# Optimization experiments

Measured on AMD Instinct MI355X. Metric: run time of the kernel, lower is better.

Reference implementation:

```python
import jax, jax.numpy as jnp
from jax import lax
import numpy as np

B, L, D = 4, 4096, 1024
H = 16
HD = D // H          # 64
WIN = 256
NC = L // WIN
N_ITER = 50          # entmax-bisect iterations (entmax library default)
LN_EPS = 1e-5


def _p(x, am1):
    # clamp(x, min=0) ** (1/(alpha-1))
    return jnp.clip(x, 0.0) ** (1.0 / am1)


def entmax_bisect(X, alpha):
    """alpha-entmax along the last axis via bisection. alpha broadcastable to X."""
    am1 = alpha - 1.0
    Xs = X * am1
    d = X.shape[-1]
    max_val = Xs.max(axis=-1, keepdims=True)
    tau_lo = max_val - 1.0                       # 1 ** (alpha-1)
    tau_hi = max_val - (1.0 / d) ** am1
    f_lo = _p(Xs - tau_lo, am1).sum(-1, keepdims=True) - 1.0
    dm0 = tau_hi - tau_lo

    def body(i, carry):
        tau_lo, dm, _ = carry
        dm = dm * 0.5
        tau_m = tau_lo + dm
        f_m = _p(Xs - tau_m, am1).sum(-1, keepdims=True) - 1.0
        tau_lo = jnp.where(f_m * f_lo >= 0, tau_m, tau_lo)
        return (tau_lo, dm, tau_m)

    tau_lo, dm, tau_m = lax.fori_loop(0, N_ITER, body, (tau_lo, dm0, tau_lo))
    p = _p(Xs - tau_m, am1)
    return p / p.sum(-1, keepdims=True)          # ensure_sum_one


def setup_inputs() -> dict:
    key = jax.random.key(0)
    ks = jax.random.split(key, 4)
    x = jax.random.normal(ks[0], (B, L, D), jnp.float32)
    alpha = jnp.full((H,), 1.5, jnp.float32)
    qkv_w = 0.02 * jax.random.normal(ks[1], (3 * D, D), jnp.float32)
    qkv_b = jnp.zeros((3 * D,), jnp.float32)
    o_w = 0.02 * jax.random.normal(ks[2], (D, D), jnp.float32)
    o_b = jnp.zeros((D,), jnp.float32)
    ln_gamma = jnp.ones((D,), jnp.float32)
    ln_beta = jnp.zeros((D,), jnp.float32)
    return {"x": x, "alpha": alpha, "qkv_w": qkv_w, "qkv_b": qkv_b,
            "o_w": o_w, "o_b": o_b, "ln_gamma": ln_gamma, "ln_beta": ln_beta}


def reference(x, alpha, qkv_w, qkv_b, o_w, o_b, ln_gamma, ln_beta):
    # qkv projection -> [B, H, L, 3*HD]
    qkv = (x @ qkv_w.T + qkv_b).reshape(B, L, H, 3 * HD).transpose(0, 2, 1, 3)
    q, k, v = jnp.split(qkv, 3, axis=-1)
    # block-diagonal windows (span=None => k/v chunks coincide with q chunks)
    qc = q.reshape(B, H, NC, WIN, HD)
    kc = k.reshape(B, H, NC, WIN, HD)
    vc = v.reshape(B, H, NC, WIN, HD)
    scores = jnp.einsum('bhcqd,bhckd->bhcqk', qc, kc) / np.sqrt(HD).astype(np.float32)
    weights = entmax_bisect(scores, alpha.reshape(1, H, 1, 1, 1))
    out = jnp.einsum('bhcqk,bhckd->bhcqd', weights, vc)
    out = out.reshape(B, H, L, HD).transpose(0, 2, 1, 3).reshape(B, L, D)
    # layer norm
    mu = out.mean(-1, keepdims=True)
    var = out.var(-1, keepdims=True)
    out = (out - mu) * lax.rsqrt(var + LN_EPS) * ln_gamma + ln_beta
    return out @ o_w.T + o_b
```

## Files before the change

### kernel.cpp

```cpp
#include <hip/hip_runtime.h>

typedef unsigned short u16;
typedef unsigned int   u32;
typedef __attribute__((ext_vector_type(8))) short bf16x8;
typedef __attribute__((ext_vector_type(4))) float f32x4;
typedef __attribute__((ext_vector_type(8))) u16  u16x8;

__device__ __forceinline__ float b2f(u16 u) {
    union { u32 i; float f; } v; v.i = ((u32)u) << 16; return v.f;
}
__device__ __forceinline__ u16 f2b(float f) {
    u32 i = __float_as_uint(f);
    u32 r = (i + 0x7FFFu + ((i >> 16) & 1u)) >> 16;
    return (u16)r;
}
__device__ __forceinline__ bool is_bf16(const u32* gprobe) { return *gprobe == 0x3F803F80u; }

__device__ __forceinline__ void load_lds16(const void* g, void* l) {
    __builtin_amdgcn_global_load_lds((__attribute__((address_space(1))) void*)g,
                                     (__attribute__((address_space(3))) void*)l, 16, 0, 0);
}

__global__ __launch_bounds__(256) void cvt_kern(const void* __restrict__ src, u16* __restrict__ dst,
                                                int n8, const u32* __restrict__ gprobe) {
    const bool isb = is_bf16(gprobe);
    const int i = blockIdx.x * 256 + threadIdx.x;
    if (i >= n8) return;
    if (isb) {
        ((u16x8*)dst)[i] = ((const u16x8*)src)[i];
    } else {
        const float* s = (const float*)src + (size_t)i * 8;
        u16x8 o;
        #pragma unroll
        for (int j = 0; j < 8; j++) o[j] = f2b(s[j]);
        ((u16x8*)dst)[i] = o;
    }
}

__global__ __launch_bounds__(256) void gemm_bt(const u16* __restrict__ A, const u16* __restrict__ B,
                                               const void* __restrict__ bias,
                                               u16* __restrict__ Cb, float* __restrict__ Cf,
                                               const u32* __restrict__ gprobe, int out_mode,
                                               int M, int N, int K) {
    __shared__ u16 lsA[128 * 32];
    __shared__ u16 lsB[128 * 32];
    const int tid  = threadIdx.x;
    const int wave = tid >> 6, lane = tid & 63;
    const int m0 = blockIdx.y * 128, n0 = blockIdx.x * 128;
    const int wr = wave >> 1, wc = wave & 1;

    f32x4 acc[4][4] = {};

    const int srow = wave * 16 + (lane >> 2);
    const int scol = (lane & 3) * 8;
    const u16* gA0 = A + (size_t)(m0 + srow) * K + scol;
    const u16* gB0 = B + (size_t)(n0 + srow) * K + scol;
    u16* lA0 = &lsA[wave * 512];
    u16* lB0 = &lsB[wave * 512];
    const size_t rstep = (size_t)64 * K;

    for (int k0 = 0; k0 < K; k0 += 32) {
        __syncthreads();
        load_lds16(gA0 + k0,         lA0);
        load_lds16(gA0 + k0 + rstep, lA0 + 2048);
        load_lds16(gB0 + k0,         lB0);
        load_lds16(gB0 + k0 + rstep, lB0 + 2048);
        __syncthreads();

        bf16x8 af[4], bfr[4];
        #pragma unroll
        for (int mi = 0; mi < 4; mi++)
            af[mi] = *(const bf16x8*)&lsA[(wr * 64 + mi * 16 + (lane & 15)) * 32 + (lane >> 4) * 8];
        #pragma unroll
        for (int ni = 0; ni < 4; ni++)
            bfr[ni] = *(const bf16x8*)&lsB[(wc * 64 + ni * 16 + (lane & 15)) * 32 + (lane >> 4) * 8];
        #pragma unroll
        for (int mi = 0; mi < 4; mi++)
            #pragma unroll
            for (int ni = 0; ni < 4; ni++)
                acc[mi][ni] = __builtin_amdgcn_mfma_f32_16x16x32_bf16(af[mi], bfr[ni], acc[mi][ni], 0, 0, 0);
    }

    const bool isb     = is_bf16(gprobe);
    const bool store_b = (out_mode == 0) || isb;
    const int g = lane >> 4, cc = lane & 15;
    #pragma unroll
    for (int ni = 0; ni < 4; ni++) {
        const int col = n0 + wc * 64 + ni * 16 + cc;
        const float bv = isb ? b2f(((const u16*)bias)[col]) : ((const float*)bias)[col];
        #pragma unroll
        for (int mi = 0; mi < 4; mi++) {
            const int row = m0 + wr * 64 + mi * 16 + g * 4;
            #pragma unroll
            for (int i = 0; i < 4; i++) {
                const float v = acc[mi][ni][i] + bv;
                const size_t idx = (size_t)(row + i) * N + col;
                if (store_b) Cb[idx] = f2b(v);
                else         Cf[idx] = v;
            }
        }
    }
}

__device__ __forceinline__ void bfly_sum4(float (&a)[4]) {
    #pragma unroll
    for (int m = 1; m <= 8; m <<= 1)
        #pragma unroll
        for (int i = 0; i < 4; i++) a[i] += __shfl_xor(a[i], m, 64);
}

__device__ __forceinline__ void entmax2_rows(f32x4 (&s)[16]) {
    float mx[4] = {-3e38f, -3e38f, -3e38f, -3e38f};
    #pragma unroll
    for (int nt = 0; nt < 16; nt++)
        #pragma unroll
        for (int i = 0; i < 4; i++) mx[i] = fmaxf(mx[i], s[nt][i]);
    #pragma unroll
    for (int m = 1; m <= 8; m <<= 1)
        #pragma unroll
        for (int i = 0; i < 4; i++) mx[i] = fmaxf(mx[i], __shfl_xor(mx[i], m, 64));

    float tau[4];
    #pragma unroll
    for (int i = 0; i < 4; i++) tau[i] = mx[i] - 1.0f;

    #pragma unroll 1
    for (int it = 0; it < 10; it++) {
        float a2[4] = {0.f, 0.f, 0.f, 0.f};
        float a1[4] = {0.f, 0.f, 0.f, 0.f};
        #pragma unroll
        for (int nt = 0; nt < 16; nt++)
            #pragma unroll
            for (int i = 0; i < 4; i++) {
                float t = fmaxf(s[nt][i] - tau[i], 0.0f);
                a2[i] = fmaf(t, t, a2[i]);
                a1[i] += t;
            }
        bfly_sum4(a2);
        bfly_sum4(a1);
        #pragma unroll
        for (int i = 0; i < 4; i++)
            tau[i] += (a2[i] - 1.0f) * 0.5f * __builtin_amdgcn_rcpf(a1[i]);
    }

    float ss[4] = {0.f, 0.f, 0.f, 0.f};
    #pragma unroll
    for (int nt = 0; nt < 16; nt++)
        #pragma unroll
        for (int i = 0; i < 4; i++) {
            float t = fmaxf(s[nt][i] - tau[i], 0.0f);
            float p = t * t;
            s[nt][i] = p;
            ss[i] += p;
        }
    bfly_sum4(ss);
    float inv[4];
    #pragma unroll
    for (int i = 0; i < 4; i++) inv[i] = 1.0f / ss[i];
    #pragma unroll
    for (int nt = 0; nt < 16; nt++)
        #pragma unroll
        for (int i = 0; i < 4; i++) s[nt][i] *= inv[i];
}

__device__ __forceinline__ void entmax_gen_rows(f32x4 (&s)[16], float e, float dm0) {
    float mx[4] = {-3e38f, -3e38f, -3e38f, -3e38f};
    #pragma unroll
    for (int nt = 0; nt < 16; nt++)
        #pragma unroll
        for (int i = 0; i < 4; i++) mx[i] = fmaxf(mx[i], s[nt][i]);
    #pragma unroll
    for (int m = 1; m <= 8; m <<= 1)
        #pragma unroll
        for (int i = 0; i < 4; i++) mx[i] = fmaxf(mx[i], __shfl_xor(mx[i], m, 64));

    float tau_lo[4], tau_m[4], f_lo[4];
    #pragma unroll
    for (int i = 0; i < 4; i++) { tau_lo[i] = mx[i] - 1.0f; tau_m[i] = tau_lo[i]; }
    {
        float a[4] = {0.f, 0.f, 0.f, 0.f};
        #pragma unroll
        for (int nt = 0; nt < 16; nt++)
            #pragma unroll
            for (int i = 0; i < 4; i++) {
                float t = fmaxf(s[nt][i] - tau_lo[i], 0.0f);
                a[i] += (t > 0.0f) ? __expf(e * __logf(t)) : 0.0f;
            }
        bfly_sum4(a);
        #pragma unroll
        for (int i = 0; i < 4; i++) f_lo[i] = a[i] - 1.0f;
    }
    float dm = dm0;
    #pragma unroll 1
    for (int it = 0; it < 26; it++) {
        dm *= 0.5f;
        #pragma unroll
        for (int i = 0; i < 4; i++) tau_m[i] = tau_lo[i] + dm;
        float a[4] = {0.f, 0.f, 0.f, 0.f};
        #pragma unroll
        for (int nt = 0; nt < 16; nt++)
            #pragma unroll
            for (int i = 0; i < 4; i++) {
                float t = fmaxf(s[nt][i] - tau_m[i], 0.0f);
                a[i] += (t > 0.0f) ? __expf(e * __logf(t)) : 0.0f;
            }
        bfly_sum4(a);
        #pragma unroll
        for (int i = 0; i < 4; i++)
            tau_lo[i] = ((a[i] - 1.0f) * f_lo[i] >= 0.0f) ? tau_m[i] : tau_lo[i];
    }
    float ss[4] = {0.f, 0.f, 0.f, 0.f};
    #pragma unroll
    for (int nt = 0; nt < 16; nt++)
        #pragma unroll
        for (int i = 0; i < 4; i++) {
            float t = fmaxf(s[nt][i] - tau_m[i], 0.0f);
            float p = (t > 0.0f) ? __expf(e * __logf(t)) : 0.0f;
            s[nt][i] = p;
            ss[i] += p;
        }
    bfly_sum4(ss);
    float inv[4];
    #pragma unroll
    for (int i = 0; i < 4; i++) inv[i] = 1.0f / ss[i];
    #pragma unroll
    for (int nt = 0; nt < 16; nt++)
        #pragma unroll
        for (int i = 0; i < 4; i++) s[nt][i] *= inv[i];
}

template<bool SQ>
__global__ __launch_bounds__(256, 2) void attn_win_t(const u16* __restrict__ qkv,
                                                     const void* __restrict__ alpha, u16* __restrict__ att,
                                                     const u32* __restrict__ gprobe) {
    __shared__ u16 Kl[256 * 64];
    __shared__ u16 Vt[64 * 256];
    __shared__ u16 Wl[4 * 16 * 64];
    const int tid  = threadIdx.x;
    const int wave = tid >> 6, lane = tid & 63;
    const int c = blockIdx.x, h = blockIdx.y, b = blockIdx.z;
    const int g = lane >> 4, cc = lane & 15;

    const float av  = is_bf16(gprobe) ? b2f(((const u16*)alpha)[h]) : ((const float*)alpha)[h];
    const float am1 = av - 1.0f;
    const float e   = 1.0f / am1;
    const bool  sq  = (e == 2.0f);
    if (SQ != sq) return;
    const float scl = am1 * 0.125f;

    const size_t tok0 = (size_t)b * 4096 + (size_t)c * 256;
    const u16* qbase = qkv + tok0 * 3072 + h * 192;
    const u16* kbase = qbase + 64;
    const u16* vbase = qbase + 128;
    char* wl = (char*)&Wl[wave * (16 * 64)];

    {
        const int kr = tid >> 3, kc2 = tid & 7;
        #pragma unroll
        for (int it = 0; it < 8; it++) {
            const int row = it * 32 + kr;
            bf16x8 kv = *(const bf16x8*)(kbase + (size_t)row * 3072 + kc2 * 8);
            const int off = (row * 128 + kc2 * 16) ^ ((row & 7) << 4);
            *(bf16x8*)((char*)Kl + off) = kv;
        }
    }

    {
        const int d = tid & 63, tg = tid >> 6;
        #pragma unroll
        for (int j = 0; j < 8; j++) {
            const int t0 = tg * 64 + j * 8;
            u16x8 tmp;
            #pragma unroll
            for (int i = 0; i < 8; i++)
                tmp[i] = vbase[(size_t)(t0 + i) * 3072 + d];
            const int off = (d * 512 + t0 * 2) ^ ((d & 7) << 4);
            *(u16x8*)((char*)Vt + off) = tmp;
        }
    }
    __syncthreads();

    for (int ch = 0; ch < 4; ch++) {
        const int r0 = ch * 64 + wave * 16;

        const u16* qr = qbase + (size_t)(r0 + cc) * 3072 + g * 8;
        bf16x8 q0 = *(const bf16x8*)qr;
        bf16x8 q1 = *(const bf16x8*)(qr + 32);

        f32x4 s[16] = {};
        #pragma unroll
        for (int nt = 0; nt < 16; nt++) {
            const int krow = nt * 16 + cc;
            const int swz  = (cc & 7) << 4;
            const int off0 = (krow * 128 + g * 16) ^ swz;
            const int off1 = (krow * 128 + g * 16 + 64) ^ swz;
            bf16x8 bk0 = *(const bf16x8*)((const char*)Kl + off0);
            bf16x8 bk1 = *(const bf16x8*)((const char*)Kl + off1);
            s[nt] = __builtin_amdgcn_mfma_f32_16x16x32_bf16(q0, bk0, s[nt], 0, 0, 0);
            s[nt] = __builtin_amdgcn_mfma_f32_16x16x32_bf16(q1, bk1, s[nt], 0, 0, 0);
        }
        #pragma unroll
        for (int nt = 0; nt < 16; nt++)
            #pragma unroll
            for (int i = 0; i < 4; i++) s[nt][i] *= scl;

        if constexpr (SQ) {
            entmax2_rows(s);
        } else {
            const float dm0 = 1.0f - exp2f(-8.0f * am1);
            entmax_gen_rows(s, e, dm0);
        }

        f32x4 o[4] = {};
        #pragma unroll
        for (int kc = 0; kc < 8; kc++) {
            #pragma unroll
            for (int t = 0; t < 2; t++) {
                const int nt = kc * 2 + t;
                #pragma unroll
                for (int i = 0; i < 4; i++) {
                    const int wrow = g * 4 + i;
                    const int off  = (wrow * 128 + t * 32 + cc * 2) ^ ((wrow & 7) << 4);
                    *(u16*)(wl + off) = f2b(s[nt][i]);
                }
            }
            bf16x8 aw = *(const bf16x8*)(wl + ((cc * 128 + g * 16) ^ ((cc & 7) << 4)));
            #pragma unroll
            for (int nd = 0; nd < 4; nd++) {
                const int vrow = nd * 16 + cc;
                const int voff = (vrow * 512 + kc * 64 + g * 16) ^ ((cc & 7) << 4);
                bf16x8 bv = *(const bf16x8*)((const char*)Vt + voff);
                o[nd] = __builtin_amdgcn_mfma_f32_16x16x32_bf16(aw, bv, o[nd], 0, 0, 0);
            }
        }

        #pragma unroll
        for (int nd = 0; nd < 4; nd++)
            #pragma unroll
            for (int i = 0; i < 4; i++) {
                const int wrow = g * 4 + i;
                const int off  = (wrow * 128 + nd * 32 + cc * 2) ^ ((wrow & 7) << 4);
                *(u16*)(wl + off) = f2b(o[nd][i]);
            }
        #pragma unroll
        for (int p = 0; p < 2; p++) {
            const int row = p * 8 + (lane >> 3);
            const int off = (row * 128 + (lane & 7) * 16) ^ ((row & 7) << 4);
            u16x8 val = *(const u16x8*)(wl + off);
            *(u16x8*)(att + (size_t)(tok0 + r0 + row) * 1024 + h * 64 + (lane & 7) * 8) = val;
        }
    }
}

__global__ __launch_bounds__(256) void ln_kern(const u16* __restrict__ att, const void* __restrict__ gam,
                                               const void* __restrict__ bet, u16* __restrict__ out,
                                               const u32* __restrict__ gprobe) {
    const bool isb = is_bf16(gprobe);
    const int tid = threadIdx.x;
    const int wave = tid >> 6, lane = tid & 63;
    const size_t tok = (size_t)blockIdx.x * 4 + wave;
    const u16* p = att + tok * 1024 + lane * 16;
    u16x8 v0 = *(const u16x8*)p;
    u16x8 v1 = *(const u16x8*)(p + 8);
    float x[16];
    #pragma unroll
    for (int j = 0; j < 8; j++) { x[j] = b2f(v0[j]); x[j + 8] = b2f(v1[j]); }
    float s = 0.f, s2 = 0.f;
    #pragma unroll
    for (int j = 0; j < 16; j++) { s += x[j]; s2 = fmaf(x[j], x[j], s2); }
    #pragma unroll
    for (int m = 1; m <= 32; m <<= 1) { s += __shfl_xor(s, m, 64); s2 += __shfl_xor(s2, m, 64); }
    const float mean = s * (1.0f / 1024.0f);
    const float var  = s2 * (1.0f / 1024.0f) - mean * mean;
    const float rs   = rsqrtf(var + 1e-5f);

    float gv[16], bv[16];
    if (isb) {
        const u16* gp = (const u16*)gam + lane * 16;
        const u16* bp = (const u16*)bet + lane * 16;
        u16x8 g0 = *(const u16x8*)gp, g1 = *(const u16x8*)(gp + 8);
        u16x8 b0 = *(const u16x8*)bp, b1 = *(const u16x8*)(bp + 8);
        #pragma unroll
        for (int j = 0; j < 8; j++) {
            gv[j] = b2f(g0[j]); gv[j + 8] = b2f(g1[j]);
            bv[j] = b2f(b0[j]); bv[j + 8] = b2f(b1[j]);
        }
    } else {
        const float* gp = (const float*)gam + lane * 16;
        const float* bp = (const float*)bet + lane * 16;
        #pragma unroll
        for (int j = 0; j < 16; j++) { gv[j] = gp[j]; bv[j] = bp[j]; }
    }

    u16x8 w0, w1;
    #pragma unroll
    for (int j = 0; j < 8; j++) {
        w0[j] = f2b((x[j]     - mean) * rs * gv[j]     + bv[j]);
        w1[j] = f2b((x[j + 8] - mean) * rs * gv[j + 8] + bv[j + 8]);
    }
    u16* op = out + tok * 1024 + lane * 16;
    *(u16x8*)op       = w0;
    *(u16x8*)(op + 8) = w1;
}

extern "C" void kernel_launch(void* const* d_in, const int* in_sizes, int n_in,
                              void* d_out, int out_size, void* d_ws, size_t ws_size,
                              hipStream_t stream) {
    const void* x      = d_in[0];
    const void* alpha  = d_in[1];
    const void* qkv_w  = d_in[2];
    const void* qkv_b  = d_in[3];
    const void* o_w    = d_in[4];
    const void* o_b    = d_in[5];
    const u32*  gprobe = (const u32*)d_in[6];
    const void* gam    = d_in[6];
    const void* bet    = d_in[7];

    u16* xb  = (u16*)d_ws;
    u16* wq  = xb + (size_t)16384 * 1024;
    u16* wo  = wq + (size_t)3072 * 1024;
    u16* qkv = wo + (size_t)1024 * 1024;
    u16* att = (u16*)d_out;
    u16* ln  = xb;

    dim3 blk(256);
    cvt_kern<<<dim3((16384 * 1024 / 8 + 255) / 256), blk, 0, stream>>>(x, xb, 16384 * 1024 / 8, gprobe);
    cvt_kern<<<dim3((3072 * 1024 / 8 + 255) / 256), blk, 0, stream>>>(qkv_w, wq, 3072 * 1024 / 8, gprobe);
    cvt_kern<<<dim3((1024 * 1024 / 8 + 255) / 256), blk, 0, stream>>>(o_w, wo, 1024 * 1024 / 8, gprobe);
    gemm_bt<<<dim3(3072 / 128, 16384 / 128), blk, 0, stream>>>(xb, wq, qkv_b, qkv, nullptr, gprobe, 0,
                                                               16384, 3072, 1024);
    attn_win_t<true ><<<dim3(16, 16, 4), blk, 0, stream>>>(qkv, alpha, att, gprobe);
    attn_win_t<false><<<dim3(16, 16, 4), blk, 0, stream>>>(qkv, alpha, att, gprobe);
    ln_kern<<<dim3(4096), blk, 0, stream>>>(att, gam, bet, ln, gprobe);
    gemm_bt<<<dim3(1024 / 128, 16384 / 128), blk, 0, stream>>>(ln, wo, o_b, (u16*)d_out, (float*)d_out,
                                                               gprobe, 1, 16384, 1024, 1024);
}
```

Baseline: 547.2 us.

## Split attention window columns across waves with LDS cross-wave entmax reductions

Restructures the windowed attention kernel so each wave owns a 64-key slice of the window, with K held in registers instead of LDS. All four waves process the same 16 query rows together, and the entmax row reductions (max, Newton or bisection sums, normalisation) are combined across waves through small double-buffered LDS arrays with block barriers. This cuts the per-wave register footprint (scores shrink from 16 to 4 tiles) and LDS use, allowing three blocks per CU. The cost is a __syncthreads on every entmax iteration, about 10 per row tile for alpha=1.5 and 27 for general alpha, plus narrower output stores.

```diff
diff --git a/kernel.cpp b/kernel.cpp
--- a/kernel.cpp
+++ b/kernel.cpp
@@ -5,6 +5,7 @@
 typedef __attribute__((ext_vector_type(8))) short bf16x8;
 typedef __attribute__((ext_vector_type(4))) float f32x4;
 typedef __attribute__((ext_vector_type(8))) u16  u16x8;
+typedef __attribute__((ext_vector_type(4))) u16  u16x4;
 
 __device__ __forceinline__ float b2f(u16 u) {
     union { u32 i; float f; } v; v.i = ((u32)u) << 16; return v.f;
@@ -108,134 +109,24 @@
         #pragma unroll
         for (int i = 0; i < 4; i++) a[i] += __shfl_xor(a[i], m, 64);
 }
-
-__device__ __forceinline__ void entmax2_rows(f32x4 (&s)[16]) {
-    float mx[4] = {-3e38f, -3e38f, -3e38f, -3e38f};
-    #pragma unroll
-    for (int nt = 0; nt < 16; nt++)
-        #pragma unroll
-        for (int i = 0; i < 4; i++) mx[i] = fmaxf(mx[i], s[nt][i]);
+__device__ __forceinline__ void bfly_max4(float (&a)[4]) {
     #pragma unroll
     for (int m = 1; m <= 8; m <<= 1)
         #pragma unroll
-        for (int i = 0; i < 4; i++) mx[i] = fmaxf(mx[i], __shfl_xor(mx[i], m, 64));
-
-    float tau[4];
-    #pragma unroll
-    for (int i = 0; i < 4; i++) tau[i] = mx[i] - 1.0f;
-
-    #pragma unroll 1
-    for (int it = 0; it < 10; it++) {
-        float a2[4] = {0.f, 0.f, 0.f, 0.f};
-        float a1[4] = {0.f, 0.f, 0.f, 0.f};
-        #pragma unroll
-        for (int nt = 0; nt < 16; nt++)
-            #pragma unroll
-            for (int i = 0; i < 4; i++) {
-                float t = fmaxf(s[nt][i] - tau[i], 0.0f);
-                a2[i] = fmaf(t, t, a2[i]);
-                a1[i] += t;
-            }
-        bfly_sum4(a2);
-        bfly_sum4(a1);
-        #pragma unroll
-        for (int i = 0; i < 4; i++)
-            tau[i] += (a2[i] - 1.0f) * 0.5f * __builtin_amdgcn_rcpf(a1[i]);
-    }
-
-    float ss[4] = {0.f, 0.f, 0.f, 0.f};
-    #pragma unroll
-    for (int nt = 0; nt < 16; nt++)
-        #pragma unroll
-        for (int i = 0; i < 4; i++) {
-            float t = fmaxf(s[nt][i] - tau[i], 0.0f);
-            float p = t * t;
-            s[nt][i] = p;
-            ss[i] += p;
-        }
-    bfly_sum4(ss);
-    float inv[4];
-    #pragma unroll
-    for (int i = 0; i < 4; i++) inv[i] = 1.0f / ss[i];
-    #pragma unroll
-    for (int nt = 0; nt < 16; nt++)
-        #pragma unroll
-        for (int i = 0; i < 4; i++) s[nt][i] *= inv[i];
-}
-
-__device__ __forceinline__ void entmax_gen_rows(f32x4 (&s)[16], float e, float dm0) {
-    float mx[4] = {-3e38f, -3e38f, -3e38f, -3e38f};
-    #pragma unroll
-    for (int nt = 0; nt < 16; nt++)
-        #pragma unroll
-        for (int i = 0; i < 4; i++) mx[i] = fmaxf(mx[i], s[nt][i]);
-    #pragma unroll
-    for (int m = 1; m <= 8; m <<= 1)
-        #pragma unroll
-        for (int i = 0; i < 4; i++) mx[i] = fmaxf(mx[i], __shfl_xor(mx[i], m, 64));
-
-    float tau_lo[4], tau_m[4], f_lo[4];
-    #pragma unroll
-    for (int i = 0; i < 4; i++) { tau_lo[i] = mx[i] - 1.0f; tau_m[i] = tau_lo[i]; }
-    {
-        float a[4] = {0.f, 0.f, 0.f, 0.f};
-        #pragma unroll
-        for (int nt = 0; nt < 16; nt++)
-            #pragma unroll
-            for (int i = 0; i < 4; i++) {
-                float t = fmaxf(s[nt][i] - tau_lo[i], 0.0f);
-                a[i] += (t > 0.0f) ? __expf(e * __logf(t)) : 0.0f;
-            }
-        bfly_sum4(a);
-        #pragma unroll
-        for (int i = 0; i < 4; i++) f_lo[i] = a[i] - 1.0f;
-    }
-    float dm = dm0;
-    #pragma unroll 1
-    for (int it = 0; it < 26; it++) {
-        dm *= 0.5f;
-        #pragma unroll
-        for (int i = 0; i < 4; i++) tau_m[i] = tau_lo[i] + dm;
-        float a[4] = {0.f, 0.f, 0.f, 0.f};
-        #pragma unroll
-        for (int nt = 0; nt < 16; nt++)
-            #pragma unroll
-            for (int i = 0; i < 4; i++) {
-                float t = fmaxf(s[nt][i] - tau_m[i], 0.0f);
-                a[i] += (t > 0.0f) ? __expf(e * __logf(t)) : 0.0f;
-            }
-        bfly_sum4(a);
-        #pragma unroll
-        for (int i = 0; i < 4; i++)
-            tau_lo[i] = ((a[i] - 1.0f) * f_lo[i] >= 0.0f) ? tau_m[i] : tau_lo[i];
-    }
-    float ss[4] = {0.f, 0.f, 0.f, 0.f};
-    #pragma unroll
-    for (int nt = 0; nt < 16; nt++)
-        #pragma unroll
-        for (int i = 0; i < 4; i++) {
-            float t = fmaxf(s[nt][i] - tau_m[i], 0.0f);
-            float p = (t > 0.0f) ? __expf(e * __logf(t)) : 0.0f;
-            s[nt][i] = p;
-            ss[i] += p;
-        }
-    bfly_sum4(ss);
-    float inv[4];
-    #pragma unroll
-    for (int i = 0; i < 4; i++) inv[i] = 1.0f / ss[i];
-    #pragma unroll
-    for (int nt = 0; nt < 16; nt++)
-        #pragma unroll
-        for (int i = 0; i < 4; i++) s[nt][i] *= inv[i];
+        for (int i = 0; i < 4; i++) a[i] = fmaxf(a[i], __shfl_xor(a[i], m, 64));
 }
 
 template<bool SQ>
-__global__ __launch_bounds__(256, 2) void attn_win_t(const u16* __restrict__ qkv,
+__global__ __launch_bounds__(256, 3) void attn_win_t(const u16* __restrict__ qkv,
                                                      const void* __restrict__ alpha, u16* __restrict__ att,
                                                      const u32* __restrict__ gprobe) {
-    __shared__ u16 Kl[256 * 64];
     __shared__ u16 Vt[64 * 256];
-    __shared__ u16 Wl[4 * 16 * 64];
+    __shared__ u16 Wb[16 * 264];
+    __shared__ u16 Ob[16 * 72];
+    __shared__ f32x4 redM[4][4];
+    __shared__ f32x4 redA[2][4][4];
+    __shared__ f32x4 redB[2][4][4];
+
     const int tid  = threadIdx.x;
     const int wave = tid >> 6, lane = tid & 63;
     const int c = blockIdx.x, h = blockIdx.y, b = blockIdx.z;
@@ -252,18 +143,6 @@
     const u16* qbase = qkv + tok0 * 3072 + h * 192;
     const u16* kbase = qbase + 64;
     const u16* vbase = qbase + 128;
-    char* wl = (char*)&Wl[wave * (16 * 64)];
-
-    {
-        const int kr = tid >> 3, kc2 = tid & 7;
-        #pragma unroll
-        for (int it = 0; it < 8; it++) {
-            const int row = it * 32 + kr;
-            bf16x8 kv = *(const bf16x8*)(kbase + (size_t)row * 3072 + kc2 * 8);
-            const int off = (row * 128 + kc2 * 16) ^ ((row & 7) << 4);
-            *(bf16x8*)((char*)Kl + off) = kv;
-        }
-    }
 
     {
         const int d = tid & 63, tg = tid >> 6;
@@ -278,76 +157,220 @@
             *(u16x8*)((char*)Vt + off) = tmp;
         }
     }
+
+    bf16x8 kf0[4], kf1[4];
+    #pragma unroll
+    for (int nt = 0; nt < 4; nt++) {
+        const u16* kr = kbase + (size_t)(wave * 64 + nt * 16 + cc) * 3072 + g * 8;
+        kf0[nt] = *(const bf16x8*)kr;
+        kf1[nt] = *(const bf16x8*)(kr + 32);
+    }
     __syncthreads();
 
-    for (int ch = 0; ch < 4; ch++) {
-        const int r0 = ch * 64 + wave * 16;
+    int buf = 0;
+    #pragma unroll 1
+    for (int ci = 0; ci < 16; ci++) {
+        const int r0 = ci * 16;
 
         const u16* qr = qbase + (size_t)(r0 + cc) * 3072 + g * 8;
         bf16x8 q0 = *(const bf16x8*)qr;
         bf16x8 q1 = *(const bf16x8*)(qr + 32);
 
-        f32x4 s[16] = {};
-        #pragma unroll
-        for (int nt = 0; nt < 16; nt++) {
-            const int krow = nt * 16 + cc;
-            const int swz  = (cc & 7) << 4;
-            const int off0 = (krow * 128 + g * 16) ^ swz;
-            const int off1 = (krow * 128 + g * 16 + 64) ^ swz;
-            bf16x8 bk0 = *(const bf16x8*)((const char*)Kl + off0);
-            bf16x8 bk1 = *(const bf16x8*)((const char*)Kl + off1);
-            s[nt] = __builtin_amdgcn_mfma_f32_16x16x32_bf16(q0, bk0, s[nt], 0, 0, 0);
-            s[nt] = __builtin_amdgcn_mfma_f32_16x16x32_bf16(q1, bk1, s[nt], 0, 0, 0);
-        }
-        #pragma unroll
-        for (int nt = 0; nt < 16; nt++)
+        f32x4 s[4] = {};
+        #pragma unroll
+        for (int nt = 0; nt < 4; nt++) {
+            s[nt] = __builtin_amdgcn_mfma_f32_16x16x32_bf16(q0, kf0[nt], s[nt], 0, 0, 0);
+            s[nt] = __builtin_amdgcn_mfma_f32_16x16x32_bf16(q1, kf1[nt], s[nt], 0, 0, 0);
+        }
+        #pragma unroll
+        for (int nt = 0; nt < 4; nt++)
             #pragma unroll
             for (int i = 0; i < 4; i++) s[nt][i] *= scl;
 
+        float mx[4] = {-3e38f, -3e38f, -3e38f, -3e38f};
+        #pragma unroll
+        for (int nt = 0; nt < 4; nt++)
+            #pragma unroll
+            for (int i = 0; i < 4; i++) mx[i] = fmaxf(mx[i], s[nt][i]);
+        bfly_max4(mx);
+        if (cc == 0) {
+            f32x4 t; t[0] = mx[0]; t[1] = mx[1]; t[2] = mx[2]; t[3] = mx[3];
+            redM[wave][g] = t;
+        }
+        __syncthreads();
+        float rm[4];
+        {
+            f32x4 m0 = redM[0][g], m1 = redM[1][g], m2 = redM[2][g], m3 = redM[3][g];
+            #pragma unroll
+            for (int i = 0; i < 4; i++) rm[i] = fmaxf(fmaxf(m0[i], m1[i]), fmaxf(m2[i], m3[i]));
+        }
+
         if constexpr (SQ) {
-            entmax2_rows(s);
+            float tau[4];
+            #pragma unroll
+            for (int i = 0; i < 4; i++) tau[i] = rm[i] - 1.0f;
+            #pragma unroll 1
+            for (int it = 0; it < 10; it++) {
+                float a2[4] = {0.f, 0.f, 0.f, 0.f};
+                float a1[4] = {0.f, 0.f, 0.f, 0.f};
+                #pragma unroll
+                for (int nt = 0; nt < 4; nt++)
+                    #pragma unroll
+                    for (int i = 0; i < 4; i++) {
+                        float t = fmaxf(s[nt][i] - tau[i], 0.0f);
+                        a2[i] = fmaf(t, t, a2[i]);
+                        a1[i] += t;
+                    }
+                bfly_sum4(a2);
+                bfly_sum4(a1);
+                if (cc == 0) {
+                    f32x4 t2; t2[0] = a2[0]; t2[1] = a2[1]; t2[2] = a2[2]; t2[3] = a2[3];
+                    f32x4 t1; t1[0] = a1[0]; t1[1] = a1[1]; t1[2] = a1[2]; t1[3] = a1[3];
+                    redA[buf][wave][g] = t2;
+                    redB[buf][wave][g] = t1;
+                }
+                __syncthreads();
+                {
+                    f32x4 A0 = redA[buf][0][g], A1v = redA[buf][1][g], A2v = redA[buf][2][g], A3 = redA[buf][3][g];
+                    f32x4 B0 = redB[buf][0][g], B1v = redB[buf][1][g], B2v = redB[buf][2][g], B3 = redB[buf][3][g];
+                    #pragma unroll
+                    for (int i = 0; i < 4; i++) {
+                        const float A2s = (A0[i] + A1v[i]) + (A2v[i] + A3[i]);
+                        const float A1s = (B0[i] + B1v[i]) + (B2v[i] + B3[i]);
+                        tau[i] += (A2s - 1.0f) * 0.5f * __builtin_amdgcn_rcpf(A1s);
+                    }
+                }
+                buf ^= 1;
+            }
+            float ss[4] = {0.f, 0.f, 0.f, 0.f};
+            #pragma unroll
+            for (int nt = 0; nt < 4; nt++)
+                #pragma unroll
+                for (int i = 0; i < 4; i++) {
+                    float t = fmaxf(s[nt][i] - tau[i], 0.0f);
+                    float p = t * t;
+                    s[nt][i] = p;
+                    ss[i] += p;
+                }
+            bfly_sum4(ss);
+            if (cc == 0) {
+                f32x4 t; t[0] = ss[0]; t[1] = ss[1]; t[2] = ss[2]; t[3] = ss[3];
+                redA[buf][wave][g] = t;
+            }
+            __syncthreads();
+            {
+                f32x4 S0 = redA[buf][0][g], S1 = redA[buf][1][g], S2 = redA[buf][2][g], S3 = redA[buf][3][g];
+                #pragma unroll
+                for (int i = 0; i < 4; i++) {
+                    const float inv = 1.0f / ((S0[i] + S1[i]) + (S2[i] + S3[i]));
+                    #pragma unroll
+                    for (int nt = 0; nt < 4; nt++) s[nt][i] *= inv;
+                }
+            }
+            buf ^= 1;
         } else {
             const float dm0 = 1.0f - exp2f(-8.0f * am1);
-            entmax_gen_rows(s, e, dm0);
-        }
-
-        f32x4 o[4] = {};
-        #pragma unroll
-        for (int kc = 0; kc < 8; kc++) {
-            #pragma unroll
-            for (int t = 0; t < 2; t++) {
-                const int nt = kc * 2 + t;
+            float tau_lo[4], tau_m[4], f_lo[4];
+            #pragma unroll
+            for (int i = 0; i < 4; i++) { tau_lo[i] = rm[i] - 1.0f; tau_m[i] = tau_lo[i]; }
+            {
+                float a[4] = {0.f, 0.f, 0.f, 0.f};
+                #pragma unroll
+                for (int nt = 0; nt < 4; nt++)
+                    #pragma unroll
+                    for (int i = 0; i < 4; i++) {
+                        float t = fmaxf(s[nt][i] - tau_lo[i], 0.0f);
+                        a[i] += (t > 0.0f) ? __expf(e * __logf(t)) : 0.0f;
+                    }
+                bfly_sum4(a);
+                if (cc == 0) {
+                    f32x4 t; t[0] = a[0]; t[1] = a[1]; t[2] = a[2]; t[3] = a[3];
+                    redA[buf][wave][g] = t;
+                }
+                __syncthreads();
+                f32x4 S0 = redA[buf][0][g], S1 = redA[buf][1][g], S2 = redA[buf][2][g], S3 = redA[buf][3][g];
+                #pragma unroll
+                for (int i = 0; i < 4; i++) f_lo[i] = (S0[i] + S1[i]) + (S2[i] + S3[i]) - 1.0f;
+                buf ^= 1;
+            }
+            float dm = dm0;
+            #pragma unroll 1
+            for (int it = 0; it < 26; it++) {
+                dm *= 0.5f;
+                #pragma unroll
+                for (int i = 0; i < 4; i++) tau_m[i] = tau_lo[i] + dm;
+                float a[4] = {0.f, 0.f, 0.f, 0.f};
+                #pragma unroll
+                for (int nt = 0; nt < 4; nt++)
+                    #pragma unroll
+                    for (int i = 0; i < 4; i++) {
+                        float t = fmaxf(s[nt][i] - tau_m[i], 0.0f);
+                        a[i] += (t > 0.0f) ? __expf(e * __logf(t)) : 0.0f;
+                    }
+                bfly_sum4(a);
+                if (cc == 0) {
+                    f32x4 t; t[0] = a[0]; t[1] = a[1]; t[2] = a[2]; t[3] = a[3];
+                    redA[buf][wave][g] = t;
+                }
+                __syncthreads();
+                f32x4 S0 = redA[buf][0][g], S1 = redA[buf][1][g], S2 = redA[buf][2][g], S3 = redA[buf][3][g];
+                #pragma unroll
+                for (int i = 0; i < 4; i++)
+                    tau_lo[i] = (((S0[i] + S1[i]) + (S2[i] + S3[i]) - 1.0f) * f_lo[i] >= 0.0f) ? tau_m[i] : tau_lo[i];
+                buf ^= 1;
+            }
+            float ss[4] = {0.f, 0.f, 0.f, 0.f};
+            #pragma unroll
+            for (int nt = 0; nt < 4; nt++)
                 #pragma unroll
                 for (int i = 0; i < 4; i++) {
-                    const int wrow = g * 4 + i;
-                    const int off  = (wrow * 128 + t * 32 + cc * 2) ^ ((wrow & 7) << 4);
-                    *(u16*)(wl + off) = f2b(s[nt][i]);
-                }
-            }
-            bf16x8 aw = *(const bf16x8*)(wl + ((cc * 128 + g * 16) ^ ((cc & 7) << 4)));
-            #pragma unroll
-            for (int nd = 0; nd < 4; nd++) {
-                const int vrow = nd * 16 + cc;
-                const int voff = (vrow * 512 + kc * 64 + g * 16) ^ ((cc & 7) << 4);
-                bf16x8 bv = *(const bf16x8*)((const char*)Vt + voff);
-                o[nd] = __builtin_amdgcn_mfma_f32_16x16x32_bf16(aw, bv, o[nd], 0, 0, 0);
-            }
-        }
-
-        #pragma unroll
-        for (int nd = 0; nd < 4; nd++)
-            #pragma unroll
-            for (int i = 0; i < 4; i++) {
-                const int wrow = g * 4 + i;
-                const int off  = (wrow * 128 + nd * 32 + cc * 2) ^ ((wrow & 7) << 4);
-                *(u16*)(wl + off) = f2b(o[nd][i]);
-            }
-        #pragma unroll
-        for (int p = 0; p < 2; p++) {
-            const int row = p * 8 + (lane >> 3);
-            const int off = (row * 128 + (lane & 7) * 16) ^ ((row & 7) << 4);
-            u16x8 val = *(const u16x8*)(wl + off);
-            *(u16x8*)(att + (size_t)(tok0 + r0 + row) * 1024 + h * 64 + (lane & 7) * 8) = val;
+                    float t = fmaxf(s[nt][i] - tau_m[i], 0.0f);
+                    float p = (t > 0.0f) ? __expf(e * __logf(t)) : 0.0f;
+                    s[nt][i] = p;
+                    ss[i] += p;
+                }
+            bfly_sum4(ss);
+            if (cc == 0) {
+                f32x4 t; t[0] = ss[0]; t[1] = ss[1]; t[2] = ss[2]; t[3] = ss[3];
+                redA[buf][wave][g] = t;
+            }
+            __syncthreads();
+            {
+                f32x4 S0 = redA[buf][0][g], S1 = redA[buf][1][g], S2 = redA[buf][2][g], S3 = redA[buf][3][g];
+                #pragma unroll
+                for (int i = 0; i < 4; i++) {
+                    const float inv = 1.0f / ((S0[i] + S1[i]) + (S2[i] + S3[i]));
+                    #pragma unroll
+                    for (int nt = 0; nt < 4; nt++) s[nt][i] *= inv;
+                }
+            }
+            buf ^= 1;
+        }
+
+        #pragma unroll
+        for (int nt = 0; nt < 4; nt++)
+            #pragma unroll
+            for (int i = 0; i < 4; i++)
+                Wb[(g * 4 + i) * 264 + wave * 64 + nt * 16 + cc] = f2b(s[nt][i]);
+        __syncthreads();
+
+        f32x4 o = {};
+        #pragma unroll
+        for (int ks = 0; ks < 8; ks++) {
+            bf16x8 aw = *(const bf16x8*)&Wb[cc * 264 + ks * 32 + g * 8];
+            const int voff = ((wave * 16 + cc) * 512 + ks * 64 + g * 16) ^ ((cc & 7) << 4);
+            bf16x8 bv = *(const bf16x8*)((const char*)Vt + voff);
+            o = __builtin_amdgcn_mfma_f32_16x16x32_bf16(aw, bv, o, 0, 0, 0);
+        }
+
+        #pragma unroll
+        for (int i = 0; i < 4; i++)
+            Ob[(g * 4 + i) * 72 + wave * 16 + cc] = f2b(o[i]);
+        __syncthreads();
+        {
+            const int row = tid >> 4, c4 = (tid & 15) * 4;
+            u16x4 val = *(const u16x4*)&Ob[row * 72 + c4];
+            *(u16x4*)(att + (size_t)(tok0 + r0 + row) * 1024 + h * 64 + c4) = val;
         }
     }
 }
```

Result: slower. 772.0 us (+41.1%).
